# Optimization experiments

Measured on AMD Instinct MI355X. Metric: run time of the kernel, lower is better.

Reference implementation:

```python
import jax, jax.numpy as jnp
import numpy as np

N, E, F_IN = 50000, 800000, 128
H1, C1 = 4, 32          # layer 1: heads, channels (concat -> 128)
H2, C2 = 1, 40          # layer 2: out heads, num_class (mean over heads)
NEG_SLOPE = 0.2


def setup_inputs() -> dict:
    key = jax.random.key(0)
    ks = jax.random.split(key, 10)
    x = jax.random.normal(ks[0], (N, F_IN), dtype=jnp.float32)
    edge_index = jax.random.randint(ks[1], (2, E), 0, N, dtype=jnp.int32)
    s1 = 1.0 / np.sqrt(F_IN)
    s2 = 1.0 / np.sqrt(H1 * C1)
    W1 = jax.random.normal(ks[2], (F_IN, H1 * C1), dtype=jnp.float32) * s1
    att_src1 = jax.random.normal(ks[3], (H1, C1), dtype=jnp.float32) * s1
    att_dst1 = jax.random.normal(ks[4], (H1, C1), dtype=jnp.float32) * s1
    b1 = jnp.zeros((H1 * C1,), dtype=jnp.float32)
    W2 = jax.random.normal(ks[5], (H1 * C1, H2 * C2), dtype=jnp.float32) * s2
    att_src2 = jax.random.normal(ks[6], (H2, C2), dtype=jnp.float32) * s2
    att_dst2 = jax.random.normal(ks[7], (H2, C2), dtype=jnp.float32) * s2
    b2 = jnp.zeros((C2,), dtype=jnp.float32)
    return {"x": x, "edge_index": edge_index, "W1": W1, "att_src1": att_src1,
            "att_dst1": att_dst1, "b1": b1, "W2": W2, "att_src2": att_src2,
            "att_dst2": att_dst2, "b2": b2}


def _gat_layer(x, src, dst, W, a_src, a_dst, b, concat):
    # PyG GATConv (eval): linear -> per-head attention logits on edges ->
    # segment-softmax over each destination's in-edges -> scatter-aggregate.
    n = x.shape[0]
    Hh, C = a_src.shape
    h = (x @ W).reshape(n, Hh, C)                       # [N,H,C]
    al_s = jnp.sum(h * a_src, axis=-1)                  # [N,H]
    al_d = jnp.sum(h * a_dst, axis=-1)                  # [N,H]
    alpha = jax.nn.leaky_relu(al_s[src] + al_d[dst], NEG_SLOPE)  # [E,H]
    m = jax.lax.stop_gradient(jax.ops.segment_max(alpha, dst, num_segments=n))
    e = jnp.exp(alpha - m[dst])
    denom = jax.ops.segment_sum(e, dst, num_segments=n)
    a = e / (denom[dst] + 1e-16)                        # [E,H]
    out = jax.ops.segment_sum(h[src] * a[..., None], dst, num_segments=n)
    out = out.reshape(n, Hh * C) if concat else out.mean(axis=1)
    return out + b


def reference(x, edge_index, W1, att_src1, att_dst1, b1, W2, att_src2, att_dst2, b2):
    n = x.shape[0]
    loop = jnp.arange(n, dtype=edge_index.dtype)        # GATConv add_self_loops=True
    src = jnp.concatenate([edge_index[0], loop])
    dst = jnp.concatenate([edge_index[1], loop])
    h = _gat_layer(x, src, dst, W1, att_src1, att_dst1, b1, concat=True)
    h = jax.nn.elu(h)
    out = _gat_layer(h, src, dst, W2, att_src2, att_dst2, b2, concat=False)
    return out
```

## Files before the change

kernel.cpp:

```cpp
#include <hip/hip_runtime.h>
#include <hip/hip_bf16.h>
#include <hip/hip_fp16.h>
#include <math.h>

constexpr int N_NODES = 50000;
constexpr int E_EDGES = 800000;
constexpr float NEG_SLOPE = 0.2f;
constexpr int CAP = 64;
constexpr int G1_BLOCKS   = (N_NODES + 63) / 64;
constexpr int LINK_BLOCKS = (E_EDGES + 255) / 256;

typedef _Float16 half8 __attribute__((ext_vector_type(8)));
typedef _Float16 half2v __attribute__((ext_vector_type(2)));
typedef float    floatx4 __attribute__((ext_vector_type(4)));

static inline int cdiv(long long a, int b) { return (int)((a + b - 1) / b); }

__device__ inline float leaky(float a) { return a > 0.f ? a : NEG_SLOPE * a; }
__device__ inline unsigned pack2h(float a, float b) {
    union { _Float16 h[2]; unsigned u; } p;
    p.h[0] = (_Float16)a; p.h[1] = (_Float16)b; return p.u;
}
__device__ inline float2 unp2h(unsigned u) {
    __half2 hh = *reinterpret_cast<__half2*>(&u);
    return __half22float2(hh);
}
__device__ inline float sel4(const float4& v, int h) {
    float a = (h & 2) ? v.z : v.x;
    float b = (h & 2) ? v.w : v.y;
    return (h & 1) ? b : a;
}

__global__ __launch_bounds__(256) void gemm1_link_kernel(const float* __restrict__ x,
                                                         const float* __restrict__ W,
                                                         const float* __restrict__ as1,
                                                         const float* __restrict__ ad1,
                                                         unsigned short* __restrict__ h1h,
                                                         float* __restrict__ als,
                                                         float* __restrict__ ald,
                                                         const int* __restrict__ ei,
                                                         int* __restrict__ head_,
                                                         int2* __restrict__ next2) {
    __shared__ _Float16 xS[64 * 136];
    __shared__ _Float16 wtS[128 * 72];
    __shared__ float asld[128], adld[128];
    int t = threadIdx.x;

    if (blockIdx.x >= G1_BLOCKS) {
        int e = (blockIdx.x - G1_BLOCKS) * 256 + t;
        if (e < E_EDGES) {
            int s = ei[e], d = ei[E_EDGES + e];
            int old = atomicExch(&head_[d], e);
            next2[e] = make_int2(s, old);
        }
        return;
    }

    int row0 = blockIdx.x * 64;
    if (t < 128) { asld[t] = as1[t]; adld[t] = ad1[t]; }
    #pragma unroll
    for (int i = 0; i < 8; ++i) {
        int fi = i * 256 + t;
        int r = fi >> 5, c4 = (fi & 31) * 4;
        int gr = row0 + r;
        float4 v = make_float4(0.f, 0.f, 0.f, 0.f);
        if (gr < N_NODES) v = *(const float4*)&x[(size_t)gr * 128 + c4];
        union { _Float16 h[4]; uint2 u; } pk;
        pk.h[0] = (_Float16)v.x; pk.h[1] = (_Float16)v.y;
        pk.h[2] = (_Float16)v.z; pk.h[3] = (_Float16)v.w;
        *(uint2*)&xS[r * 136 + c4] = pk.u;
    }

    int w = t >> 6, lane = t & 63, quad = lane >> 4, l16 = lane & 15;
    floatx4 z = {0.f, 0.f, 0.f, 0.f};
    floatx4 c[4][2];
    #pragma unroll
    for (int rt = 0; rt < 4; ++rt) { c[rt][0] = z; c[rt][1] = z; }

    #pragma unroll
    for (int kc = 0; kc < 2; ++kc) {
        __syncthreads();
        #pragma unroll
        for (int i = 0; i < 4; ++i) {
            int fi = i * 256 + t;
            int kp = fi & 31, nq = fi >> 5;
            int krow = kc * 64 + 2 * kp;
            float4 va = *(const float4*)&W[(size_t)krow * 128 + nq * 4];
            float4 vb = *(const float4*)&W[(size_t)(krow + 1) * 128 + nq * 4];
            *(unsigned*)&wtS[(nq * 4 + 0) * 72 + 2 * kp] = pack2h(va.x, vb.x);
            *(unsigned*)&wtS[(nq * 4 + 1) * 72 + 2 * kp] = pack2h(va.y, vb.y);
            *(unsigned*)&wtS[(nq * 4 + 2) * 72 + 2 * kp] = pack2h(va.z, vb.z);
            *(unsigned*)&wtS[(nq * 4 + 3) * 72 + 2 * kp] = pack2h(va.w, vb.w);
        }
        __syncthreads();
        #pragma unroll
        for (int ks2 = 0; ks2 < 2; ++ks2) {
            int ko = ks2 * 32 + quad * 8;
            half8 b0 = *(const half8*)&wtS[(w * 32 + l16) * 72 + ko];
            half8 b1 = *(const half8*)&wtS[(w * 32 + 16 + l16) * 72 + ko];
            #pragma unroll
            for (int rt = 0; rt < 4; ++rt) {
                half8 a = *(const half8*)&xS[(rt * 16 + l16) * 136 + kc * 64 + ko];
                c[rt][0] = __builtin_amdgcn_mfma_f32_16x16x32_f16(a, b0, c[rt][0], 0, 0, 0);
                c[rt][1] = __builtin_amdgcn_mfma_f32_16x16x32_f16(a, b1, c[rt][1], 0, 0, 0);
            }
        }
    }
    __syncthreads();
    _Float16* cbuf = wtS;
    #pragma unroll
    for (int rt = 0; rt < 4; ++rt)
        #pragma unroll
        for (int ctl = 0; ctl < 2; ++ctl)
            #pragma unroll
            for (int reg = 0; reg < 4; ++reg)
                cbuf[(rt * 16 + quad * 4 + reg) * 136 + (w * 32 + ctl * 16 + l16)]
                    = (_Float16)c[rt][ctl][reg];
    __syncthreads();
    int r = t >> 2, hq = t & 3;
    int n = row0 + r;
    if (n < N_NODES) {
        float ps = 0.f, pd = 0.f;
        #pragma unroll
        for (int i = 0; i < 4; ++i) {
            uint4 uv = *(uint4*)&cbuf[r * 136 + hq * 32 + i * 8];
            *(uint4*)&h1h[(size_t)n * 128 + hq * 32 + i * 8] = uv;
            union { uint4 u; _Float16 h[8]; } cv; cv.u = uv;
            #pragma unroll
            for (int k = 0; k < 8; ++k) {
                float v = (float)cv.h[k];
                ps += v * asld[hq * 32 + i * 8 + k];
                pd += v * adld[hq * 32 + i * 8 + k];
            }
        }
        als[n * 4 + hq] = ps;
        ald[n * 4 + hq] = pd;
    }
}

__global__ __launch_bounds__(256) void traverse_fixed_kernel(const int* __restrict__ head,
                                                             const int2* __restrict__ next2,
                                                             unsigned short* __restrict__ csr16,
                                                             int* __restrict__ deg) {
    int d = blockIdx.x * 256 + threadIdx.x;
    if (d >= N_NODES) return;
    int base = d * CAP;
    csr16[base] = (unsigned short)d;
    int c = 1;
    int e = head[d];
    while (e >= 0 && c < CAP) {
        int2 v = next2[e];
        csr16[base + c] = (unsigned short)v.x;
        e = v.y;
        ++c;
    }
    deg[d] = c;
}

__global__ __launch_bounds__(256) void agg1_kernel(const int* __restrict__ deg_,
                                                   const unsigned short* __restrict__ csr16,
                                                   const float* __restrict__ als,
                                                   const float4* __restrict__ ald4,
                                                   const unsigned short* __restrict__ h1h,
                                                   const float* __restrict__ b1,
                                                   unsigned short* __restrict__ out1h) {
    int wv   = threadIdx.x >> 6;
    int lane = threadIdx.x & 63;
    int half = lane >> 5;
    int l    = lane & 31;
    int myhead = l >> 3;
    int we   = lane & 15;
    int wh   = lane >> 4;
    int d    = blockIdx.x * 4 + wv;
    int dg   = deg_[d];
    int base = d * CAP;
    float4 aldd = ald4[d];
    float d_hw = sel4(aldd, wh);

    float sm = 0.f;
    float acc[4] = {0.f, 0.f, 0.f, 0.f};
    int sfirst = (int)csr16[base];
    for (int j = 0; j < dg; j += 16) {
        int s_w = (int)csr16[base + j + we];
        float av = als[s_w * 4 + wh];
        float wgt = (j + we < dg) ? __expf(leaky(av + d_hw)) : 0.f;
        uint4 blkA = *(const uint4*)&csr16[base + j];
        uint4 blkB = *(const uint4*)&csr16[base + j + 8];
        unsigned bw[8] = { blkA.x, blkA.y, blkA.z, blkA.w,
                           blkB.x, blkB.y, blkB.z, blkB.w };
        int ss[8];
        #pragma unroll
        for (int p = 0; p < 8; ++p) {
            unsigned b = __builtin_amdgcn_readfirstlane(bw[p]);
            int e0 = (int)(b & 0xffff), e1 = (int)(b >> 16);
            int mys = half ? e1 : e0;
            if (j + 2 * p + half >= dg) mys = sfirst;
            ss[p] = mys;
        }
        uint2 hv[8];
        #pragma unroll
        for (int p = 0; p < 8; ++p)
            hv[p] = *(const uint2*)(h1h + ((size_t)ss[p] << 7) + 4 * l);
        float ww[8];
        #pragma unroll
        for (int p = 0; p < 8; ++p) {
            ww[p] = __shfl(wgt, 16 * myhead + 2 * p + half);
            sm += ww[p];
        }
        half2v hacc0 = { (_Float16)0.f, (_Float16)0.f };
        half2v hacc1 = { (_Float16)0.f, (_Float16)0.f };
        #pragma unroll
        for (int p = 0; p < 8; ++p) {
            half2v v0 = *reinterpret_cast<half2v*>(&hv[p].x);
            half2v v1 = *reinterpret_cast<half2v*>(&hv[p].y);
            _Float16 hw = (_Float16)ww[p];
            half2v hwv = { hw, hw };
            hacc0 += v0 * hwv;
            hacc1 += v1 * hwv;
        }
        acc[0] += (float)hacc0[0]; acc[1] += (float)hacc0[1];
        acc[2] += (float)hacc1[0]; acc[3] += (float)hacc1[1];
    }
    sm += __shfl_xor(sm, 32);
    #pragma unroll
    for (int k = 0; k < 4; ++k) acc[k] += __shfl_xor(acc[k], 32);
    if (half == 0) {
        float inv = 1.f / (sm + 1e-16f);
        float v[4];
        #pragma unroll
        for (int k = 0; k < 4; ++k) {
            v[k] = acc[k] * inv + b1[4 * l + k];
            v[k] = v[k] > 0.f ? v[k] : __expf(v[k]) - 1.f;
        }
        uint2 o;
        o.x = pack2h(v[0], v[1]);
        o.y = pack2h(v[2], v[3]);
        *(uint2*)&out1h[(size_t)d * 128 + 4 * l] = o;
    }
}

__global__ __launch_bounds__(256) void gemm2_kernel(const unsigned short* __restrict__ out1h,
                                                    const float* __restrict__ W2,
                                                    const float* __restrict__ as2,
                                                    const float* __restrict__ ad2,
                                                    unsigned short* __restrict__ h2h,
                                                    float* __restrict__ als,
                                                    float* __restrict__ ald) {
    __shared__ _Float16 aS[64 * 136];
    __shared__ _Float16 wt2[48 * 136];
    __shared__ float asld[40], adld[40];
    int t = threadIdx.x;
    int row0 = blockIdx.x * 64;
    if (t < 40) { asld[t] = as2[t]; adld[t] = ad2[t]; }
    #pragma unroll
    for (int i = 0; i < 4; ++i) {
        int fi = i * 256 + t;
        int r = fi >> 4, s8 = (fi & 15) * 8;
        int gr = row0 + r;
        uint4 v = make_uint4(0u, 0u, 0u, 0u);
        if (gr < N_NODES) v = *(const uint4*)&out1h[(size_t)gr * 128 + s8];
        *(uint4*)&aS[r * 136 + s8] = v;
    }
    #pragma unroll
    for (int i = 0; i < 3; ++i) {
        int fi = i * 256 + t;
        if (fi < 640) {
            int kp = fi & 63, nq = fi >> 6;
            float4 va = *(const float4*)&W2[(size_t)(2 * kp) * 40 + nq * 4];
            float4 vb = *(const float4*)&W2[(size_t)(2 * kp + 1) * 40 + nq * 4];
            *(unsigned*)&wt2[(nq * 4 + 0) * 136 + 2 * kp] = pack2h(va.x, vb.x);
            *(unsigned*)&wt2[(nq * 4 + 1) * 136 + 2 * kp] = pack2h(va.y, vb.y);
            *(unsigned*)&wt2[(nq * 4 + 2) * 136 + 2 * kp] = pack2h(va.z, vb.z);
            *(unsigned*)&wt2[(nq * 4 + 3) * 136 + 2 * kp] = pack2h(va.w, vb.w);
        }
    }
    __syncthreads();

    int w = t >> 6, lane = t & 63, quad = lane >> 4, l16 = lane & 15;
    floatx4 z = {0.f, 0.f, 0.f, 0.f};
    floatx4 c0 = z, c1 = z, c2 = z;
    #pragma unroll
    for (int ks = 0; ks < 4; ++ks) {
        int ko = ks * 32 + quad * 8;
        half8 a  = *(const half8*)&aS[(w * 16 + l16) * 136 + ko];
        half8 b0 = *(const half8*)&wt2[(l16) * 136 + ko];
        half8 b1 = *(const half8*)&wt2[(16 + l16) * 136 + ko];
        half8 b2 = *(const half8*)&wt2[(32 + l16) * 136 + ko];
        c0 = __builtin_amdgcn_mfma_f32_16x16x32_f16(a, b0, c0, 0, 0, 0);
        c1 = __builtin_amdgcn_mfma_f32_16x16x32_f16(a, b1, c1, 0, 0, 0);
        c2 = __builtin_amdgcn_mfma_f32_16x16x32_f16(a, b2, c2, 0, 0, 0);
    }
    __syncthreads();
    #pragma unroll
    for (int reg = 0; reg < 4; ++reg) {
        int rr = (w * 16 + quad * 4 + reg) * 136;
        aS[rr + l16]      = (_Float16)c0[reg];
        aS[rr + 16 + l16] = (_Float16)c1[reg];
        aS[rr + 32 + l16] = (_Float16)c2[reg];
    }
    __syncthreads();
    for (int fi = t; fi < 320; fi += 256) {
        int r = fi / 5, s = fi - r * 5;
        int n = row0 + r;
        if (n < N_NODES) {
            uint4 v = *(uint4*)&aS[r * 136 + s * 8];
            *(uint4*)&h2h[(size_t)n * 40 + s * 8] = v;
        }
    }
    int r = t >> 2, q = t & 3;
    int n = row0 + r;
    float ps = 0.f, pd = 0.f;
    #pragma unroll
    for (int i = 0; i < 10; ++i) {
        int cc = q * 10 + i;
        float v = (float)aS[r * 136 + cc];
        ps += v * asld[cc]; pd += v * adld[cc];
    }
    ps += __shfl_xor(ps, 1); ps += __shfl_xor(ps, 2);
    pd += __shfl_xor(pd, 1); pd += __shfl_xor(pd, 2);
    if (q == 0 && n < N_NODES) { als[n] = ps; ald[n] = pd; }
}

__global__ __launch_bounds__(256) void agg2_kernel(const int* __restrict__ deg_,
                                                   const unsigned short* __restrict__ csr16,
                                                   const float* __restrict__ als,
                                                   const float* __restrict__ ald,
                                                   const unsigned short* __restrict__ h2h,
                                                   const float* __restrict__ b2,
                                                   float* __restrict__ out) {
    int wv   = threadIdx.x >> 6;
    int lane = threadIdx.x & 63;
    int d    = blockIdx.x * 4 + wv;
    int dg   = deg_[d];
    int base = d * CAP;
    float aldd = ald[d];

    int slot = lane / 20;
    int idx  = lane - slot * 20;
    int sfirst = (int)csr16[base];
    float sm = 0.f, acc0 = 0.f, acc1 = 0.f;
    if (lane < 60) {
        for (int jb = 0; jb < dg; jb += 12) {
            int ss[4]; unsigned hv[4]; float ww[4];
            #pragma unroll
            for (int i = 0; i < 4; ++i) {
                int jj = jb + slot + 3 * i;
                ss[i] = (jj < dg) ? (int)csr16[base + jj] : sfirst;
            }
            #pragma unroll
            for (int i = 0; i < 4; ++i)
                hv[i] = *(const unsigned*)(h2h + (size_t)ss[i] * 40 + 2 * idx);
            #pragma unroll
            for (int i = 0; i < 4; ++i) {
                int jj = jb + slot + 3 * i;
                float w = __expf(leaky(als[ss[i]] + aldd));
                ww[i] = (jj < dg) ? w : 0.f;
            }
            #pragma unroll
            for (int i = 0; i < 4; ++i) {
                float2 f = unp2h(hv[i]);
                acc0 += f.x * ww[i]; acc1 += f.y * ww[i]; sm += ww[i];
            }
        }
    }
    float s1 = __shfl(sm,   idx + 20), s2 = __shfl(sm,   idx + 40);
    float t0 = __shfl(acc0, idx + 20), t1 = __shfl(acc0, idx + 40);
    float u0 = __shfl(acc1, idx + 20), u1 = __shfl(acc1, idx + 40);
    sm += s1 + s2; acc0 += t0 + t1; acc1 += u0 + u1;
    if (lane < 20) {
        float inv = 1.f / (sm + 1e-16f);
        float2 o = make_float2(acc0 * inv + b2[2 * lane], acc1 * inv + b2[2 * lane + 1]);
        *(float2*)&out[(size_t)d * 40 + 2 * lane] = o;
    }
}

constexpr size_t OFF_H1H    = 0;
constexpr size_t OFF_OUT1   = 3200000;
constexpr size_t OFF_ALS1   = 6400000;
constexpr size_t OFF_ALD1   = 6600000;
constexpr size_t OFF_HEAD   = 6800000;
constexpr size_t OFF_DEG    = 6860000;
constexpr size_t OFF_CSRF   = 6920000;
constexpr size_t OFF_NEXT2  = 8520000;
constexpr size_t WS_FLOATS  = 10120000;

extern "C" void kernel_launch(void* const* d_in, const int* in_sizes, int n_in,
                              void* d_out, int out_size, void* d_ws, size_t ws_size,
                              hipStream_t stream) {
    const float* x   = (const float*)d_in[0];
    const int*   ei  = (const int*)  d_in[1];
    const float* W1  = (const float*)d_in[2];
    const float* as1 = (const float*)d_in[3];
    const float* ad1 = (const float*)d_in[4];
    const float* b1  = (const float*)d_in[5];
    const float* W2  = (const float*)d_in[6];
    const float* as2 = (const float*)d_in[7];
    const float* ad2 = (const float*)d_in[8];
    const float* b2  = (const float*)d_in[9];
    float* out = (float*)d_out;

    if (ws_size < WS_FLOATS * sizeof(float)) return;

    float* ws = (float*)d_ws;
    unsigned short* h1h   = (unsigned short*)(ws + OFF_H1H);
    unsigned short* h2h   = (unsigned short*)(ws + OFF_H1H);
    unsigned short* out1h = (unsigned short*)(ws + OFF_OUT1);
    float* als1    = ws + OFF_ALS1;
    float* ald1    = ws + OFF_ALD1;
    float* als2    = ws + OFF_ALS1;
    float* ald2    = ws + OFF_ALD1;
    int*   head    = (int*)(ws + OFF_HEAD);
    int*   deg     = (int*)(ws + OFF_DEG);
    unsigned short* csr16 = (unsigned short*)(ws + OFF_CSRF);
    int2*  next2   = (int2*)(ws + OFF_NEXT2);

    int ngrid = cdiv(N_NODES, 256);

    hipMemsetAsync(head, 0xFF, (size_t)N_NODES * sizeof(int), stream);
    gemm1_link_kernel<<<G1_BLOCKS + LINK_BLOCKS, 256, 0, stream>>>(
        x, W1, as1, ad1, h1h, als1, ald1, ei, head, next2);
    traverse_fixed_kernel<<<ngrid, 256, 0, stream>>>(head, next2, csr16, deg);

    agg1_kernel<<<N_NODES / 4, 256, 0, stream>>>(deg, csr16, als1,
                                                 (const float4*)ald1,
                                                 h1h, b1, out1h);

    gemm2_kernel<<<cdiv(N_NODES, 64), 256, 0, stream>>>(out1h, W2, as2, ad2, h2h, als2, ald2);
    agg2_kernel<<<N_NODES / 4, 256, 0, stream>>>(deg, csr16, als2, ald2, h2h, b2, out);
}
```

Baseline: 221.3 us.

## Build bucketed CSR via atomicAdd slots, drop linked-list traverse, read weights directly

Replaces the linked-list edge construction (atomicExch head plus next pointers) and the separate traversal kernel with direct atomicAdd slot allocation into the fixed-capacity CSR buckets, writing the self-loop entry from the GEMM blocks. This removes one kernel launch and the pointer-chasing traversal. Both GEMM kernels now load weight fragments straight from global memory into registers instead of staging transposed weights in shared memory, which cuts LDS use and allows higher occupancy (launch bounds raised). The trade-off is atomic contention on deg, scattered global weight loads, and a neighbor order that now depends on atomic arrival.

Measured after the change: 205.6 us. -7.1%, faster.

```diff
diff --git a/kernel.cpp b/kernel.cpp
--- a/kernel.cpp
+++ b/kernel.cpp
@@ -31,18 +31,17 @@
     return (h & 1) ? b : a;
 }
 
-__global__ __launch_bounds__(256) void gemm1_link_kernel(const float* __restrict__ x,
-                                                         const float* __restrict__ W,
-                                                         const float* __restrict__ as1,
-                                                         const float* __restrict__ ad1,
-                                                         unsigned short* __restrict__ h1h,
-                                                         float* __restrict__ als,
-                                                         float* __restrict__ ald,
-                                                         const int* __restrict__ ei,
-                                                         int* __restrict__ head_,
-                                                         int2* __restrict__ next2) {
+__global__ __launch_bounds__(256, 8) void gemm1_link_kernel(const float* __restrict__ x,
+                                                            const float* __restrict__ W,
+                                                            const float* __restrict__ as1,
+                                                            const float* __restrict__ ad1,
+                                                            unsigned short* __restrict__ h1h,
+                                                            float* __restrict__ als,
+                                                            float* __restrict__ ald,
+                                                            const int* __restrict__ ei,
+                                                            int* __restrict__ deg,
+                                                            unsigned short* __restrict__ csr16) {
     __shared__ _Float16 xS[64 * 136];
-    __shared__ _Float16 wtS[128 * 72];
     __shared__ float asld[128], adld[128];
     int t = threadIdx.x;
 
@@ -50,8 +49,8 @@
         int e = (blockIdx.x - G1_BLOCKS) * 256 + t;
         if (e < E_EDGES) {
             int s = ei[e], d = ei[E_EDGES + e];
-            int old = atomicExch(&head_[d], e);
-            next2[e] = make_int2(s, old);
+            int slot = atomicAdd(&deg[d], 1) + 1;
+            if (slot < CAP) csr16[d * CAP + slot] = (unsigned short)s;
         }
         return;
     }
@@ -70,6 +69,7 @@
         pk.h[2] = (_Float16)v.z; pk.h[3] = (_Float16)v.w;
         *(uint2*)&xS[r * 136 + c4] = pk.u;
     }
+    __syncthreads();
 
     int w = t >> 6, lane = t & 63, quad = lane >> 4, l16 = lane & 15;
     floatx4 z = {0.f, 0.f, 0.f, 0.f};
@@ -77,37 +77,26 @@
     #pragma unroll
     for (int rt = 0; rt < 4; ++rt) { c[rt][0] = z; c[rt][1] = z; }
 
-    #pragma unroll
-    for (int kc = 0; kc < 2; ++kc) {
-        __syncthreads();
-        #pragma unroll
-        for (int i = 0; i < 4; ++i) {
-            int fi = i * 256 + t;
-            int kp = fi & 31, nq = fi >> 5;
-            int krow = kc * 64 + 2 * kp;
-            float4 va = *(const float4*)&W[(size_t)krow * 128 + nq * 4];
-            float4 vb = *(const float4*)&W[(size_t)(krow + 1) * 128 + nq * 4];
-            *(unsigned*)&wtS[(nq * 4 + 0) * 72 + 2 * kp] = pack2h(va.x, vb.x);
-            *(unsigned*)&wtS[(nq * 4 + 1) * 72 + 2 * kp] = pack2h(va.y, vb.y);
-            *(unsigned*)&wtS[(nq * 4 + 2) * 72 + 2 * kp] = pack2h(va.z, vb.z);
-            *(unsigned*)&wtS[(nq * 4 + 3) * 72 + 2 * kp] = pack2h(va.w, vb.w);
-        }
-        __syncthreads();
-        #pragma unroll
-        for (int ks2 = 0; ks2 < 2; ++ks2) {
-            int ko = ks2 * 32 + quad * 8;
-            half8 b0 = *(const half8*)&wtS[(w * 32 + l16) * 72 + ko];
-            half8 b1 = *(const half8*)&wtS[(w * 32 + 16 + l16) * 72 + ko];
-            #pragma unroll
-            for (int rt = 0; rt < 4; ++rt) {
-                half8 a = *(const half8*)&xS[(rt * 16 + l16) * 136 + kc * 64 + ko];
-                c[rt][0] = __builtin_amdgcn_mfma_f32_16x16x32_f16(a, b0, c[rt][0], 0, 0, 0);
-                c[rt][1] = __builtin_amdgcn_mfma_f32_16x16x32_f16(a, b1, c[rt][1], 0, 0, 0);
-            }
-        }
-    }
-    __syncthreads();
-    _Float16* cbuf = wtS;
+    const float* wcol = W + (w * 32 + l16);
+    #pragma unroll
+    for (int ks = 0; ks < 4; ++ks) {
+        int kg = ks * 32 + quad * 8;
+        const float* wp = wcol + (size_t)kg * 128;
+        half8 b0, b1;
+        #pragma unroll
+        for (int i = 0; i < 8; ++i) {
+            b0[i] = (_Float16)wp[i * 128];
+            b1[i] = (_Float16)wp[i * 128 + 16];
+        }
+        #pragma unroll
+        for (int rt = 0; rt < 4; ++rt) {
+            half8 a = *(const half8*)&xS[(rt * 16 + l16) * 136 + kg];
+            c[rt][0] = __builtin_amdgcn_mfma_f32_16x16x32_f16(a, b0, c[rt][0], 0, 0, 0);
+            c[rt][1] = __builtin_amdgcn_mfma_f32_16x16x32_f16(a, b1, c[rt][1], 0, 0, 0);
+        }
+    }
+    __syncthreads();
+    _Float16* cbuf = xS;
     #pragma unroll
     for (int rt = 0; rt < 4; ++rt)
         #pragma unroll
@@ -120,6 +109,7 @@
     int r = t >> 2, hq = t & 3;
     int n = row0 + r;
     if (n < N_NODES) {
+        if (hq == 0) csr16[n * CAP] = (unsigned short)n;
         float ps = 0.f, pd = 0.f;
         #pragma unroll
         for (int i = 0; i < 4; ++i) {
@@ -136,25 +126,6 @@
         als[n * 4 + hq] = ps;
         ald[n * 4 + hq] = pd;
     }
-}
-
-__global__ __launch_bounds__(256) void traverse_fixed_kernel(const int* __restrict__ head,
-                                                             const int2* __restrict__ next2,
-                                                             unsigned short* __restrict__ csr16,
-                                                             int* __restrict__ deg) {
-    int d = blockIdx.x * 256 + threadIdx.x;
-    if (d >= N_NODES) return;
-    int base = d * CAP;
-    csr16[base] = (unsigned short)d;
-    int c = 1;
-    int e = head[d];
-    while (e >= 0 && c < CAP) {
-        int2 v = next2[e];
-        csr16[base + c] = (unsigned short)v.x;
-        e = v.y;
-        ++c;
-    }
-    deg[d] = c;
 }
 
 __global__ __launch_bounds__(256) void agg1_kernel(const int* __restrict__ deg_,
@@ -172,7 +143,7 @@
     int we   = lane & 15;
     int wh   = lane >> 4;
     int d    = blockIdx.x * 4 + wv;
-    int dg   = deg_[d];
+    int dg   = min(deg_[d] + 1, CAP);
     int base = d * CAP;
     float4 aldd = ald4[d];
     float d_hw = sel4(aldd, wh);
@@ -239,15 +210,14 @@
     }
 }
 
-__global__ __launch_bounds__(256) void gemm2_kernel(const unsigned short* __restrict__ out1h,
-                                                    const float* __restrict__ W2,
-                                                    const float* __restrict__ as2,
-                                                    const float* __restrict__ ad2,
-                                                    unsigned short* __restrict__ h2h,
-                                                    float* __restrict__ als,
-                                                    float* __restrict__ ald) {
+__global__ __launch_bounds__(256, 8) void gemm2_kernel(const unsigned short* __restrict__ out1h,
+                                                       const float* __restrict__ W2,
+                                                       const float* __restrict__ as2,
+                                                       const float* __restrict__ ad2,
+                                                       unsigned short* __restrict__ h2h,
+                                                       float* __restrict__ als,
+                                                       float* __restrict__ ald) {
     __shared__ _Float16 aS[64 * 136];
-    __shared__ _Float16 wt2[48 * 136];
     __shared__ float asld[40], adld[40];
     int t = threadIdx.x;
     int row0 = blockIdx.x * 64;
@@ -261,31 +231,24 @@
         if (gr < N_NODES) v = *(const uint4*)&out1h[(size_t)gr * 128 + s8];
         *(uint4*)&aS[r * 136 + s8] = v;
     }
-    #pragma unroll
-    for (int i = 0; i < 3; ++i) {
-        int fi = i * 256 + t;
-        if (fi < 640) {
-            int kp = fi & 63, nq = fi >> 6;
-            float4 va = *(const float4*)&W2[(size_t)(2 * kp) * 40 + nq * 4];
-            float4 vb = *(const float4*)&W2[(size_t)(2 * kp + 1) * 40 + nq * 4];
-            *(unsigned*)&wt2[(nq * 4 + 0) * 136 + 2 * kp] = pack2h(va.x, vb.x);
-            *(unsigned*)&wt2[(nq * 4 + 1) * 136 + 2 * kp] = pack2h(va.y, vb.y);
-            *(unsigned*)&wt2[(nq * 4 + 2) * 136 + 2 * kp] = pack2h(va.z, vb.z);
-            *(unsigned*)&wt2[(nq * 4 + 3) * 136 + 2 * kp] = pack2h(va.w, vb.w);
-        }
-    }
     __syncthreads();
 
     int w = t >> 6, lane = t & 63, quad = lane >> 4, l16 = lane & 15;
     floatx4 z = {0.f, 0.f, 0.f, 0.f};
     floatx4 c0 = z, c1 = z, c2 = z;
+    int n2 = (l16 < 8) ? 32 + l16 : 39;
     #pragma unroll
     for (int ks = 0; ks < 4; ++ks) {
-        int ko = ks * 32 + quad * 8;
-        half8 a  = *(const half8*)&aS[(w * 16 + l16) * 136 + ko];
-        half8 b0 = *(const half8*)&wt2[(l16) * 136 + ko];
-        half8 b1 = *(const half8*)&wt2[(16 + l16) * 136 + ko];
-        half8 b2 = *(const half8*)&wt2[(32 + l16) * 136 + ko];
+        int kg = ks * 32 + quad * 8;
+        const float* wp = W2 + (size_t)kg * 40;
+        half8 b0, b1, b2;
+        #pragma unroll
+        for (int i = 0; i < 8; ++i) {
+            b0[i] = (_Float16)wp[i * 40 + l16];
+            b1[i] = (_Float16)wp[i * 40 + 16 + l16];
+            b2[i] = (_Float16)wp[i * 40 + n2];
+        }
+        half8 a  = *(const half8*)&aS[(w * 16 + l16) * 136 + kg];
         c0 = __builtin_amdgcn_mfma_f32_16x16x32_f16(a, b0, c0, 0, 0, 0);
         c1 = __builtin_amdgcn_mfma_f32_16x16x32_f16(a, b1, c1, 0, 0, 0);
         c2 = __builtin_amdgcn_mfma_f32_16x16x32_f16(a, b2, c2, 0, 0, 0);
@@ -331,7 +294,7 @@
     int wv   = threadIdx.x >> 6;
     int lane = threadIdx.x & 63;
     int d    = blockIdx.x * 4 + wv;
-    int dg   = deg_[d];
+    int dg   = min(deg_[d] + 1, CAP);
     int base = d * CAP;
     float aldd = ald[d];
 
@@ -409,17 +372,15 @@
     float* ald1    = ws + OFF_ALD1;
     float* als2    = ws + OFF_ALS1;
     float* ald2    = ws + OFF_ALD1;
-    int*   head    = (int*)(ws + OFF_HEAD);
     int*   deg     = (int*)(ws + OFF_DEG);
     unsigned short* csr16 = (unsigned short*)(ws + OFF_CSRF);
-    int2*  next2   = (int2*)(ws + OFF_NEXT2);
 
     int ngrid = cdiv(N_NODES, 256);
-
-    hipMemsetAsync(head, 0xFF, (size_t)N_NODES * sizeof(int), stream);
+    (void)ngrid;
+
+    hipMemsetAsync(deg, 0, (size_t)N_NODES * sizeof(int), stream);
     gemm1_link_kernel<<<G1_BLOCKS + LINK_BLOCKS, 256, 0, stream>>>(
-        x, W1, as1, ad1, h1h, als1, ald1, ei, head, next2);
-    traverse_fixed_kernel<<<ngrid, 256, 0, stream>>>(head, next2, csr16, deg);
+        x, W1, as1, ad1, h1h, als1, ald1, ei, deg, csr16);
 
     agg1_kernel<<<N_NODES / 4, 256, 0, stream>>>(deg, csr16, als1,
                                                  (const float4*)ald1,
```
